# Kernel optimization log

Hardware: AMD Instinct MI355X
Metric: run time of the kernel (lower is better)

## Reference

```python
import jax, jax.numpy as jnp
import numpy as np

NEG = -1e7  # matches replace_masked value -10000000.0


def tree_lstm(x, graph, wx, bx, uh, bh):
    # x: (B,T,I); graph: (B,T,T); wx: (4,H,I) gates [i,f,o,u]; uh: (4,H,H)
    B, T, _ = x.shape
    H = wx.shape[1]
    # precompute input projections for all gates/timesteps: (B,T,4,H)
    xg = jnp.einsum('bti,ghi->btgh', x, wx) + bx[None, None]
    h0 = jnp.zeros((B, T, H), x.dtype)

    def step(carry, j):
        h, c = carry
        h_j = h[:, j]  # still zeros at step j, as in the original code
        i = jax.nn.sigmoid(xg[:, j, 0] + h_j @ uh[0].T + bh[0])
        o = jax.nn.sigmoid(xg[:, j, 2] + h_j @ uh[2].T + bh[2])
        u = jnp.tanh(xg[:, j, 3] + h_j @ uh[3].T + bh[3])
        # forget gate against every node's hidden state: (B,T,H)
        f = jax.nn.sigmoid(xg[:, j, 1][:, None, :] + h @ uh[1].T + bh[1])
        # masked neighbor aggregation: bmm(mask, f*c) with mask row j
        c_j = i * u + jnp.einsum('bt,bth->bh', graph[:, j], f * c)
        h_j_new = o * jnp.tanh(c_j)
        return (h.at[:, j].set(h_j_new), c.at[:, j].set(c_j)), None

    (h, c), _ = jax.lax.scan(step, (h0, jnp.zeros_like(h0)), jnp.arange(T))
    return h, c


def masked_softmax(scores, key_mask):
    # scores: (B,Q,K); key_mask: (B,K)
    scores = jnp.where(key_mask[:, None, :] > 0, scores, NEG)
    return jax.nn.softmax(scores, axis=-1)


def pool(v, mask):
    avg = jnp.sum(v * mask[:, :, None], axis=1) / jnp.sum(mask, axis=1, keepdims=True)
    mx = jnp.max(jnp.where(mask[:, :, None] > 0, v, NEG), axis=1)
    return avg, mx


def esim_forward(premises, premises_lengths, hypotheses, hypotheses_lengths,
                 lgraph, rgraph, emb,
                 enc_wx, enc_bx, enc_uh, enc_bh,
                 comp_wx, comp_bx, comp_uh, comp_bh,
                 proj_w, proj_b, cls_w1, cls_b1, cls_w2, cls_b2):
    Tp = premises.shape[1]
    Th = hypotheses.shape[1]
    p_mask = (jnp.arange(Tp)[None, :] < premises_lengths[:, None]).astype(emb.dtype)
    h_mask = (jnp.arange(Th)[None, :] < hypotheses_lengths[:, None]).astype(emb.dtype)

    emb_p = emb[premises]
    emb_h = emb[hypotheses]

    enc_p, _ = tree_lstm(emb_p, lgraph, enc_wx, enc_bx, enc_uh, enc_bh)
    enc_h, _ = tree_lstm(emb_h, rgraph, enc_wx, enc_bx, enc_uh, enc_bh)

    # soft alignment attention
    sim = jnp.einsum('bph,bqh->bpq', enc_p, enc_h)
    att_p = masked_softmax(sim, h_mask) @ enc_h                      # (B,Tp,H)
    att_h = masked_softmax(sim.transpose(0, 2, 1), p_mask) @ enc_p   # (B,Th,H)

    enh_p = jnp.concatenate([enc_p, att_p, enc_p - att_p, enc_p * att_p], axis=-1)
    enh_h = jnp.concatenate([enc_h, att_h, enc_h - att_h, enc_h * att_h], axis=-1)

    proj_p = jax.nn.relu(enh_p @ proj_w.T + proj_b)
    proj_h = jax.nn.relu(enh_h @ proj_w.T + proj_b)

    v_ai, _ = tree_lstm(proj_p, lgraph, comp_wx, comp_bx, comp_uh, comp_bh)
    v_bj, _ = tree_lstm(proj_h, rgraph, comp_wx, comp_bx, comp_uh, comp_bh)

    a_avg, a_max = pool(v_ai, p_mask)
    b_avg, b_max = pool(v_bj, h_mask)
    v = jnp.concatenate([a_avg, a_max, b_avg, b_max], axis=1)

    hid = jnp.tanh(v @ cls_w1.T + cls_b1)
    logits = hid @ cls_w2.T + cls_b2
    return logits


def setup_inputs() -> dict:
    B, T, E, H, V, C = 32, 128, 300, 300, 50000, 3
    key = jax.random.key(0)
    ks = jax.random.split(key, 20)
    premises = jax.random.randint(ks[0], (B, T), 1, V)
    premises_lengths = jax.random.randint(ks[1], (B,), T // 2, T + 1)
    hypotheses = jax.random.randint(ks[2], (B, T), 1, V)
    hypotheses_lengths = jax.random.randint(ks[3], (B,), T // 2, T + 1)
    # sparse binary adjacency (~1-2 children per node), as in dependency trees
    lgraph = (jax.random.uniform(ks[4], (B, T, T)) < 0.01).astype(jnp.float32)
    rgraph = (jax.random.uniform(ks[5], (B, T, T)) < 0.01).astype(jnp.float32)
    emb = jax.random.normal(ks[6], (V, E), jnp.float32) * 0.05
    emb = emb.at[0].set(0.0)  # padding_idx=0

    def g(k, shape, fan_in):
        return jax.random.normal(k, shape, jnp.float32) * (1.0 / np.sqrt(fan_in))

    return {
        'premises': premises, 'premises_lengths': premises_lengths,
        'hypotheses': hypotheses, 'hypotheses_lengths': hypotheses_lengths,
        'lgraph': lgraph, 'rgraph': rgraph, 'emb': emb,
        'enc_wx': g(ks[7], (4, H, E), E), 'enc_bx': jnp.zeros((4, H), jnp.float32),
        'enc_uh': g(ks[8], (4, H, H), H), 'enc_bh': jnp.zeros((4, H), jnp.float32),
        'comp_wx': g(ks[9], (4, H, H), H), 'comp_bx': jnp.zeros((4, H), jnp.float32),
        'comp_uh': g(ks[10], (4, H, H), H), 'comp_bh': jnp.zeros((4, H), jnp.float32),
        'proj_w': g(ks[11], (H, 4 * H), 4 * H), 'proj_b': jnp.zeros((H,), jnp.float32),
        'cls_w1': g(ks[12], (H, 4 * H), 4 * H), 'cls_b1': jnp.zeros((H,), jnp.float32),
        'cls_w2': g(ks[13], (C, H), H), 'cls_b2': jnp.zeros((C,), jnp.float32),
    }


def reference(premises, premises_lengths, hypotheses, hypotheses_lengths,
              lgraph, rgraph, emb,
              enc_wx, enc_bx, enc_uh, enc_bh,
              comp_wx, comp_bx, comp_uh, comp_bh,
              proj_w, proj_b, cls_w1, cls_b1, cls_w2, cls_b2):
    return esim_forward(premises, premises_lengths, hypotheses, hypotheses_lengths,
                        lgraph, rgraph, emb,
                        enc_wx, enc_bx, enc_uh, enc_bh,
                        comp_wx, comp_bx, comp_uh, comp_bh,
                        proj_w, proj_b, cls_w1, cls_b1, cls_w2, cls_b2)
```

## Files before the change

kernel.cpp:

```cpp
#include <hip/hip_runtime.h>
#include <math.h>

#define B_ 32
#define T_ 128
#define H_ 300
#define HG 1200
#define LMAX 10
#define WLCAP 8192
#define ECAP 2048
#define NEGV -10000000.0f

typedef __attribute__((ext_vector_type(8))) short bf16x8;
typedef __attribute__((ext_vector_type(4))) float f32x4;
typedef unsigned short ushort_t;

__device__ __forceinline__ float sigm(float x){ return 1.f/(1.f+expf(-x)); }

__device__ __forceinline__ unsigned short f2bf(float x){
  union { float f; unsigned int u; } c; c.f = x;
  unsigned int u = c.u;
  return (unsigned short)((u + 0x7fffu + ((u >> 16) & 1u)) >> 16);
}
__device__ __forceinline__ float bf2f(unsigned short h){
  union { unsigned int u; float f; } c; c.u = ((unsigned int)h) << 16;
  return c.f;
}

__global__ __launch_bounds__(256) void k_prep_all(
    const float* __restrict__ enc_uh, const float* __restrict__ comp_uh,
    const float* __restrict__ enc_wx, const float* __restrict__ comp_wx,
    const float* __restrict__ pw, const float* __restrict__ cw1,
    float* __restrict__ te, float* __restrict__ tc, float* __restrict__ w1t,
    ushort_t* __restrict__ WencH, ushort_t* __restrict__ WencL,
    ushort_t* __restrict__ WcompH, ushort_t* __restrict__ WcompL,
    ushort_t* __restrict__ WPH, ushort_t* __restrict__ WPL)
{
  int i = blockIdx.x*256 + threadIdx.x;
  if (i < 90000) {
    int m = i / H_, k = i - m*H_;
    te[i] = enc_uh[H_*H_ + (size_t)k*H_ + m];
    tc[i] = comp_uh[H_*H_ + (size_t)k*H_ + m];
  } else if (i < 450000) {
    int i2 = i - 90000;
    int m = i2 / H_, k = i2 - m*H_;
    w1t[i2] = cw1[(size_t)k*HG + m];
  } else if (i < 834000) {
    int i2 = i - 450000;
    int n = i2 / 320, k = i2 - n*320;
    float v = (k < 300) ? enc_wx[(size_t)n*300 + k] : 0.f;
    ushort_t h = f2bf(v);
    WencH[i2] = h; WencL[i2] = f2bf(v - bf2f(h));
  } else if (i < 1218000) {
    int i2 = i - 834000;
    int n = i2 / 320, k = i2 - n*320;
    float v = (k < 300) ? comp_wx[(size_t)n*300 + k] : 0.f;
    ushort_t h = f2bf(v);
    WcompH[i2] = h; WcompL[i2] = f2bf(v - bf2f(h));
  } else if (i < 1496400) {
    int i2 = i - 1218000;
    int n = i2 / 928, k = i2 - n*928;
    const float* r = pw + (size_t)n*HG;
    float v = 0.f;
    if (k < 300)      v = r[k] + r[600+k];
    else if (k < 600) v = r[k] - r[k+300];
    else if (k < 900) v = r[k+300];
    ushort_t h = f2bf(v);
    WPH[i2] = h; WPL[i2] = f2bf(v - bf2f(h));
  }
}

__global__ __launch_bounds__(256) void k_embed_split(const int* __restrict__ prem, const int* __restrict__ hyp,
    const float* __restrict__ emb, ushort_t* __restrict__ EH, ushort_t* __restrict__ EL)
{
  int i = blockIdx.x*256 + threadIdx.x;
  int bt = i / 320, k = i - bt*320;
  int side = bt >> 12, bt2 = bt & 4095;
  float v = 0.f;
  if (k < 300) {
    int tok = (side == 0 ? prem : hyp)[bt2];
    v = emb[(size_t)tok*H_ + k];
  }
  ushort_t h = f2bf(v);
  EH[i] = h; EL[i] = f2bf(v - bf2f(h));
}

__global__ __launch_bounds__(256) void k_h_split(const float* __restrict__ H1,
    ushort_t* __restrict__ HH, ushort_t* __restrict__ HL)
{
  int i = blockIdx.x*256 + threadIdx.x;
  int r = i / 320, k = i - r*320;
  float v = (k < 300) ? H1[(size_t)r*H_ + k] : 0.f;
  ushort_t h = f2bf(v);
  HH[i] = h; HL[i] = f2bf(v - bf2f(h));
}

__global__ __launch_bounds__(256) void k_enh_split(const float* __restrict__ H1, const float* __restrict__ ATT,
    ushort_t* __restrict__ AH, ushort_t* __restrict__ AL)
{
  int i = blockIdx.x*256 + threadIdx.x;
  int r = i / 928, k = i - r*928;
  float v = 0.f;
  if (k < 300)      v = H1[(size_t)r*H_ + k];
  else if (k < 600) v = ATT[(size_t)r*H_ + k - 300];
  else if (k < 900) { int kk = k - 600; v = H1[(size_t)r*H_ + kk] * ATT[(size_t)r*H_ + kk]; }
  ushort_t h = f2bf(v);
  AH[i] = h; AL[i] = f2bf(v - bf2f(h));
}

__global__ __launch_bounds__(256) void k_build(const float* __restrict__ lg, const float* __restrict__ rg,
    int* __restrict__ cnt_g, int* __restrict__ coff_g, int* __restrict__ eidx_g, float* __restrict__ ew_g,
    int* __restrict__ hasp_g, int* __restrict__ depth_g, int* __restrict__ maxd_g,
    int* __restrict__ lvlcnt_g, int* __restrict__ wl_g)
{
  int chain = blockIdx.x; int s = chain >> 5, b = chain & 31;
  const float* graph = (s ? rg : lg) + (size_t)b*T_*T_;
  int tid = threadIdx.x;
  __shared__ float gbuf[T_*T_];
  __shared__ int cnt[T_], coff[T_], depth[T_], hasp[T_];
  __shared__ short eidx[ECAP];
  __shared__ float ew[ECAP];
  __shared__ int lcnt[LMAX], lbase[LMAX], lppos[LMAX], lnpos[LMAX];
  __shared__ int etot_s;

  #pragma unroll
  for (int k = 0; k < 16; ++k)
    ((float4*)gbuf)[tid + k*256] = ((const float4*)graph)[tid + k*256];
  if (tid < T_) hasp[tid] = 0;
  if (tid < LMAX) { lcnt[tid] = 0; lppos[tid] = 0; lnpos[tid] = 0; }
  __syncthreads();
  if (tid < T_) {
    int j = tid, c = 0;
    const float* gr = gbuf + j*T_;
    for (int t = 0; t < j; ++t) c += (gr[t] != 0.f) ? 1 : 0;
    cnt[j] = c;
  }
  __syncthreads();
  if (tid == 0) { int a = 0; for (int j = 0; j < T_; ++j) { coff[j] = a; a += cnt[j]; } etot_s = a; }
  __syncthreads();
  if (tid < T_) {
    int j = tid, p = coff[j];
    const float* gr = gbuf + j*T_;
    for (int t = 0; t < j; ++t) {
      float g = gr[t];
      if (g != 0.f && p < ECAP) { eidx[p] = (short)t; ew[p] = g; hasp[t] = 1; ++p; }
    }
  }
  __syncthreads();
  if (tid == 0) {
    int md = 0;
    for (int j = 0; j < T_; ++j) {
      int d = 0, e0 = coff[j], e1 = coff[j] + cnt[j];
      if (e1 > ECAP) e1 = ECAP;
      for (int k = e0; k < e1; ++k) { int dd = depth[eidx[k]] + 1; d = dd > d ? dd : d; }
      depth[j] = d; md = d > md ? d : md;
    }
    maxd_g[chain] = md;
  }
  __syncthreads();
  if (tid < T_) { int L = depth[tid]; if (L < LMAX) atomicAdd(&lcnt[L], 1); }
  __syncthreads();
  if (tid < LMAX && lcnt[tid] > 0) lbase[tid] = atomicAdd(&lvlcnt_g[tid], lcnt[tid]);
  __syncthreads();
  if (tid < T_) {
    int L = depth[tid];
    if (L < LMAX) {
      int pos;
      if (hasp[tid]) { int p = atomicAdd(&lppos[L], 1); pos = p; }
      else           { int p = atomicAdd(&lnpos[L], 1); pos = lcnt[L] - 1 - p; }
      wl_g[L*WLCAP + lbase[L] + pos] = (chain << 8) | tid;
    }
  }
  int base = chain * T_;
  if (tid < T_) {
    cnt_g[base+tid] = cnt[tid]; coff_g[base+tid] = coff[tid];
    hasp_g[base+tid] = hasp[tid]; depth_g[base+tid] = depth[tid];
  }
  int etot = etot_s; if (etot > ECAP) etot = ECAP;
  for (int i = tid; i < etot; i += 256) { eidx_g[chain*ECAP + i] = eidx[i]; ew_g[chain*ECAP + i] = ew[i]; }
}

__global__ __launch_bounds__(1024) void k_level(
    const float* __restrict__ xg, const float* __restrict__ bhv, const float* __restrict__ uh1T,
    const int* __restrict__ cnt_g, const int* __restrict__ coff_g,
    const int* __restrict__ eidx_g, const float* __restrict__ ew_g,
    const int* __restrict__ hasp_g, const int* __restrict__ lvlcnt_g, const int* __restrict__ wl_g,
    int L, float* __restrict__ hout, float* __restrict__ chist, float* __restrict__ fh)
{
  int count = lvlcnt_g[L];
  int nblk = (count + 3) >> 2;
  int tid = threadIdx.x;
  __shared__ float h_s[4][H_];
  __shared__ float psum[3][4][H_];
  __shared__ int nodes[4];
  __shared__ int anyp;
  for (int blk = blockIdx.x; blk < nblk; blk += gridDim.x) {
    int base = blk * 4;
    int nn = count - base; if (nn > 4) nn = 4;
    if (tid == 0) anyp = 0;
    __syncthreads();
    if (tid < 4) {
      int pk = (tid < nn) ? wl_g[L*WLCAP + base + tid] : -1;
      nodes[tid] = pk;
      if (pk >= 0 && hasp_g[(pk >> 8)*T_ + (pk & 255)]) atomicAdd(&anyp, 1);
    }
    __syncthreads();
    for (int w = tid; w < nn*H_; w += 1024) {
      int n = w / H_, e = w - n*H_;
      int pk = nodes[n]; int chain = pk >> 8, j = pk & 255;
      size_t cb = (size_t)chain*T_*H_, xb = (size_t)chain*T_*HG;
      const float* xp = xg + xb + (size_t)j*HG;
      float x0 = xp[e], x1 = xp[H_+e], x2 = xp[2*H_+e], x3 = xp[3*H_+e];
      float iu  = sigm(x0 + bhv[e]) * tanhf(x3 + bhv[3*H_+e]);
      float og  = sigm(x2 + bhv[2*H_+e]);
      float x1b = x1 + bhv[H_+e];
      float acc = iu;
      int c0 = coff_g[chain*T_+j], c1 = c0 + cnt_g[chain*T_+j];
      const int* ei = eidx_g + chain*ECAP;
      const float* ewp = ew_g + chain*ECAP;
      for (int k = c0; k < c1; ++k) {
        int t = ei[k];
        acc += ewp[k] * sigm(x1b + fh[cb + (size_t)t*H_ + e]) * chist[cb + (size_t)t*H_ + e];
      }
      chist[cb + (size_t)j*H_ + e] = acc;
      float hv = og * tanhf(acc);
      hout[cb + (size_t)j*H_ + e] = hv;
      h_s[n][e] = hv;
    }
    __syncthreads();
    if (anyp > 0) {
      if (tid < 3*H_) {
        int g = tid / H_, e = tid - g*H_;
        float a0=0.f, a1=0.f, a2=0.f, a3=0.f;
        const float* up = uh1T + e;
        int m0 = g*100, m1 = m0 + 100;
        #pragma unroll 4
        for (int m = m0; m < m1; ++m) {
          float u = up[(size_t)m*H_];
          a0 = fmaf(u, h_s[0][m], a0);
          a1 = fmaf(u, h_s[1][m], a1);
          a2 = fmaf(u, h_s[2][m], a2);
          a3 = fmaf(u, h_s[3][m], a3);
        }
        psum[g][0][e]=a0; psum[g][1][e]=a1; psum[g][2][e]=a2; psum[g][3][e]=a3;
      }
      __syncthreads();
      for (int w = tid; w < nn*H_; w += 1024) {
        int n = w / H_, e = w - n*H_;
        int pk = nodes[n]; int chain = pk >> 8, j = pk & 255;
        if (hasp_g[chain*T_+j]) {
          size_t cb = (size_t)chain*T_*H_;
          fh[cb + (size_t)j*H_ + e] = psum[0][n][e] + psum[1][n][e] + psum[2][n][e];
        }
      }
    }
    __syncthreads();
  }
}

__global__ __launch_bounds__(320) void k_tail(const float* __restrict__ xg, const float* __restrict__ bhv,
    const float* __restrict__ uh1T, const int* __restrict__ cnt_g, const int* __restrict__ coff_g,
    const int* __restrict__ eidx_g, const float* __restrict__ ew_g, const int* __restrict__ hasp_g,
    const int* __restrict__ depth_g, const int* __restrict__ maxd_g,
    float* __restrict__ hout, float* __restrict__ chist, float* __restrict__ fh)
{
  int chain = blockIdx.x;
  if (maxd_g[chain] < LMAX) return;
  int tid = threadIdx.x;
  bool act = tid < H_;
  float bh0=0.f,bh1=0.f,bh2=0.f,bh3=0.f;
  if (act) { bh0=bhv[tid]; bh1=bhv[H_+tid]; bh2=bhv[2*H_+tid]; bh3=bhv[3*H_+tid]; }
  __shared__ float h_lds[H_];
  size_t cb = (size_t)chain*T_*H_, xb = (size_t)chain*T_*HG;
  const int* ei = eidx_g + chain*ECAP;
  const float* ewp = ew_g + chain*ECAP;
  for (int j = 0; j < T_; ++j) {
    if (depth_g[chain*T_+j] < LMAX) continue;
    if (act) {
      const float* xp = xg + xb + (size_t)j*HG;
      float x0 = xp[tid], x1 = xp[H_+tid], x2 = xp[2*H_+tid], x3 = xp[3*H_+tid];
      float acc = sigm(x0+bh0) * tanhf(x3+bh3);
      float og  = sigm(x2+bh2);
      float x1b = x1 + bh1;
      int c0 = coff_g[chain*T_+j], c1 = c0 + cnt_g[chain*T_+j];
      for (int k = c0; k < c1; ++k) {
        int t = ei[k];
        acc += ewp[k] * sigm(x1b + fh[cb + (size_t)t*H_ + tid]) * chist[cb + (size_t)t*H_ + tid];
      }
      chist[cb + (size_t)j*H_ + tid] = acc;
      float hv = og * tanhf(acc);
      hout[cb + (size_t)j*H_ + tid] = hv;
      h_lds[tid] = hv;
    }
    __syncthreads();
    if (hasp_g[chain*T_+j] && act) {
      float a = 0.f;
      const float* up = uh1T + tid;
      #pragma unroll 4
      for (int m = 0; m < H_; ++m) a = fmaf(up[(size_t)m*H_], h_lds[m], a);
      fh[cb + (size_t)j*H_ + tid] = a;
    }
    __syncthreads();
  }
}

template<int OUTBF>
__global__ __launch_bounds__(256) void k_gemm_bf(
    const ushort_t* __restrict__ Ah, const ushort_t* __restrict__ Al, int AS,
    const ushort_t* __restrict__ Wh, const ushort_t* __restrict__ Wl, int WS,
    const float* __restrict__ bias, float* __restrict__ C,
    ushort_t* __restrict__ Ch, ushort_t* __restrict__ Cl, int CS,
    int N, int NT, int act)
{
  __shared__ ushort_t sAh[128*32], sAl[128*32], sWh[128*32], sWl[128*32];
  int tid = threadIdx.x;
  int bn = blockIdx.x * 128, bm = blockIdx.y * 128;
  int lane = tid & 63, wave = tid >> 6;
  int wr = (wave >> 1) * 64, wc = (wave & 1) * 64;
  int lrow = lane & 15, q = lane >> 4;

  int srow = tid >> 1, half = tid & 1;
  int ssw = (srow >> 1) & 3;
  int sg0 = ((2*half) ^ ssw) * 8, sg1 = ((2*half+1) ^ ssw) * 8;
  int sbase = srow * 32;
  const ushort_t* pAh = Ah + (size_t)(bm + srow)*AS + half*16;
  const ushort_t* pAl = Al + (size_t)(bm + srow)*AS + half*16;
  int wrow = bn + srow;
  int wsafe = (wrow < N) ? wrow : 0;
  const ushort_t* pWh = Wh + (size_t)wsafe*WS + half*16;
  const ushort_t* pWl = Wl + (size_t)wsafe*WS + half*16;

  bf16x8 rA0, rA1, rAl0, rAl1, rW0, rW1, rWl0, rWl1;
  auto issue = [&](int t){
    int kb = t * 32;
    rA0  = *(const bf16x8*)(pAh + kb); rA1  = *(const bf16x8*)(pAh + kb + 8);
    rAl0 = *(const bf16x8*)(pAl + kb); rAl1 = *(const bf16x8*)(pAl + kb + 8);
    rW0  = *(const bf16x8*)(pWh + kb); rW1  = *(const bf16x8*)(pWh + kb + 8);
    rWl0 = *(const bf16x8*)(pWl + kb); rWl1 = *(const bf16x8*)(pWl + kb + 8);
  };
  auto commit = [&](){
    *(bf16x8*)&sAh[sbase + sg0] = rA0; *(bf16x8*)&sAh[sbase + sg1] = rA1;
    *(bf16x8*)&sAl[sbase + sg0] = rAl0; *(bf16x8*)&sAl[sbase + sg1] = rAl1;
    *(bf16x8*)&sWh[sbase + sg0] = rW0; *(bf16x8*)&sWh[sbase + sg1] = rW1;
    *(bf16x8*)&sWl[sbase + sg0] = rWl0; *(bf16x8*)&sWl[sbase + sg1] = rWl1;
  };

  f32x4 acc[4][4];
  #pragma unroll
  for (int m = 0; m < 4; ++m)
    #pragma unroll
    for (int n = 0; n < 4; ++n) acc[m][n] = (f32x4){0.f,0.f,0.f,0.f};

  issue(0); commit();
  __syncthreads();
  for (int t = 0; t < NT; ++t) {
    bool more = (t+1 < NT);
    if (more) issue(t+1);
    bf16x8 ah[4], al[4], bh[4], bl[4];
    #pragma unroll
    for (int m = 0; m < 4; ++m) {
      int R = wr + m*16 + lrow;
      int o = R*32 + ((q ^ ((R>>1)&3)) * 8);
      ah[m] = *(const bf16x8*)&sAh[o];
      al[m] = *(const bf16x8*)&sAl[o];
    }
    #pragma unroll
    for (int n = 0; n < 4; ++n) {
      int R = wc + n*16 + lrow;
      int o = R*32 + ((q ^ ((R>>1)&3)) * 8);
      bh[n] = *(const bf16x8*)&sWh[o];
      bl[n] = *(const bf16x8*)&sWl[o];
    }
    #pragma unroll
    for (int m = 0; m < 4; ++m)
      #pragma unroll
      for (int n = 0; n < 4; ++n) {
        acc[m][n] = __builtin_amdgcn_mfma_f32_16x16x32_bf16(ah[m], bh[n], acc[m][n], 0,0,0);
        acc[m][n] = __builtin_amdgcn_mfma_f32_16x16x32_bf16(ah[m], bl[n], acc[m][n], 0,0,0);
        acc[m][n] = __builtin_amdgcn_mfma_f32_16x16x32_bf16(al[m], bh[n], acc[m][n], 0,0,0);
      }
    __syncthreads();
    if (more) commit();
    __syncthreads();
  }
  #pragma unroll
  for (int m = 0; m < 4; ++m) {
    int row0 = bm + wr + m*16 + (lane >> 4)*4;
    #pragma unroll
    for (int n = 0; n < 4; ++n) {
      int col = bn + wc + n*16 + lrow;
      if (OUTBF) {
        if (col < CS) {
          float bv = (col < N) ? bias[col] : 0.f;
          #pragma unroll
          for (int r = 0; r < 4; ++r) {
            float v = 0.f;
            if (col < N) { v = acc[m][n][r] + bv; if (act) v = fmaxf(v, 0.f); }
            ushort_t h = f2bf(v);
            Ch[(size_t)(row0 + r)*CS + col] = h;
            Cl[(size_t)(row0 + r)*CS + col] = f2bf(v - bf2f(h));
          }
        }
      } else {
        if (col < N) {
          float bv = bias[col];
          #pragma unroll
          for (int r = 0; r < 4; ++r) {
            float v = acc[m][n][r] + bv;
            if (act) v = fmaxf(v, 0.f);
            C[(size_t)(row0 + r)*N + col] = v;
          }
        }
      }
    }
  }
}

__global__ __launch_bounds__(256) void k_attn_mfma(
    const ushort_t* __restrict__ HH, const ushort_t* __restrict__ HL,
    const int* __restrict__ plen, const int* __restrict__ hlen,
    float* __restrict__ ATT)
{
  __shared__ float regA_f[12800];
  __shared__ ushort_t pbuf[2*64*136];
  ushort_t* regA = (ushort_t*)regA_f;

  int tid = threadIdx.x;
  int lane = tid & 63, wave = tid >> 6;
  int lrow = lane & 15, koff = (lane >> 4) * 8;
  int d = blockIdx.x, b = blockIdx.y, q0 = blockIdx.z * 64;
  int qbase = (d*B_ + b)*T_ + q0;
  int kbase = ((1-d)*B_ + b)*T_;
  float* outp = ATT + ((size_t)(d*B_ + b)*T_ + q0) * H_;
  int klen = (d == 0) ? hlen[b] : plen[b];

  ushort_t* sQh = regA;
  ushort_t* sQl = regA + 2560;
  ushort_t* sKh = regA + 5120;
  ushort_t* sKl = regA + 10240;
  int qrow = tid >> 2, qo = (tid & 3) * 8;
  int krow = tid >> 1, ko = (tid & 1) * 16;
  const ushort_t* Qh = HH + (size_t)(qbase + qrow)*320 + qo;
  const ushort_t* Ql = HL + (size_t)(qbase + qrow)*320 + qo;
  const ushort_t* Kh = HH + (size_t)(kbase + krow)*320 + ko;
  const ushort_t* Kl = HL + (size_t)(kbase + krow)*320 + ko;

  bf16x8 rqh, rql, rkh0, rkh1, rkl0, rkl1;
  auto issue1 = [&](int t){
    int kb = t*32;
    rqh  = *(const bf16x8*)(Qh + kb);
    rql  = *(const bf16x8*)(Ql + kb);
    rkh0 = *(const bf16x8*)(Kh + kb); rkh1 = *(const bf16x8*)(Kh + kb + 8);
    rkl0 = *(const bf16x8*)(Kl + kb); rkl1 = *(const bf16x8*)(Kl + kb + 8);
  };
  auto commit1 = [&](){
    *(bf16x8*)&sQh[qrow*40 + qo] = rqh;
    *(bf16x8*)&sQl[qrow*40 + qo] = rql;
    *(bf16x8*)&sKh[krow*40 + ko] = rkh0; *(bf16x8*)&sKh[krow*40 + ko + 8] = rkh1;
    *(bf16x8*)&sKl[krow*40 + ko] = rkl0; *(bf16x8*)&sKl[krow*40 + ko + 8] = rkl1;
  };

  f32x4 acc1[4][2];
  #pragma unroll
  for (int m = 0; m < 4; ++m)
    #pragma unroll
    for (int n = 0; n < 2; ++n) acc1[m][n] = (f32x4){0.f,0.f,0.f,0.f};
  int wc = wave * 32;

  issue1(0); commit1();
  __syncthreads();
  for (int t = 0; t < 10; ++t) {
    bool more = (t < 9);
    bf16x8 ah[4], al[4], bh[2], bl[2];
    #pragma unroll
    for (int m = 0; m < 4; ++m) {
      int o = (m*16 + lrow)*40 + koff;
      ah[m] = *(const bf16x8*)&sQh[o];
      al[m] = *(const bf16x8*)&sQl[o];
    }
    #pragma unroll
    for (int n = 0; n < 2; ++n) {
      int o = (wc + n*16 + lrow)*40 + koff;
      bh[n] = *(const bf16x8*)&sKh[o];
      bl[n] = *(const bf16x8*)&sKl[o];
    }
    if (more) issue1(t+1);
    __syncthreads();
    if (more) commit1();
    #pragma unroll
    for (int m = 0; m < 4; ++m)
      #pragma unroll
      for (int n = 0; n < 2; ++n) {
        acc1[m][n] = __builtin_amdgcn_mfma_f32_16x16x32_bf16(ah[m], bh[n], acc1[m][n], 0,0,0);
        acc1[m][n] = __builtin_amdgcn_mfma_f32_16x16x32_bf16(ah[m], bl[n], acc1[m][n], 0,0,0);
        acc1[m][n] = __builtin_amdgcn_mfma_f32_16x16x32_bf16(al[m], bh[n], acc1[m][n], 0,0,0);
      }
    __syncthreads();
  }
  float* sim = regA_f;
  #pragma unroll
  for (int m = 0; m < 4; ++m)
    #pragma unroll
    for (int n = 0; n < 2; ++n)
      #pragma unroll
      for (int r = 0; r < 4; ++r)
        sim[(m*16 + (lane>>4)*4 + r)*132 + wc + n*16 + lrow] = acc1[m][n][r];
  __syncthreads();

  {
    int row = tid >> 2, qtr = (tid & 3) * 32;
    const float* sr = sim + row*132;
    float mx = NEGV;
    for (int c = 0; c < 32; ++c) { int cg = qtr + c; float s = (cg < klen) ? sr[cg] : NEGV; mx = fmaxf(mx, s); }
    mx = fmaxf(mx, __shfl_xor(mx, 1));
    mx = fmaxf(mx, __shfl_xor(mx, 2));
    float sum = 0.f;
    for (int c = 0; c < 32; ++c) { int cg = qtr + c; if (cg < klen) sum += expf(sr[cg] - mx); }
    sum += __shfl_xor(sum, 1);
    sum += __shfl_xor(sum, 2);
    float rinv = 1.f / sum;
    for (int c = 0; c < 32; ++c) {
      int cg = qtr + c;
      float p = (cg < klen) ? expf(sr[cg] - mx) * rinv : 0.f;
      ushort_t h = f2bf(p);
      pbuf[row*136 + cg] = h;
      pbuf[64*136 + row*136 + cg] = f2bf(p - bf2f(h));
    }
  }
  __syncthreads();

  ushort_t* kth = regA;
  ushort_t* ktl = regA + 12800;
  int wr2 = (wave & 1) * 32;
  int wcf = (wave >> 1) * 160;
  f32x4 acc3[2][10];
  #pragma unroll
  for (int m = 0; m < 2; ++m)
    #pragma unroll
    for (int n = 0; n < 10; ++n) acc3[m][n] = (f32x4){0.f,0.f,0.f,0.f};
  int skey = tid >> 3, sf8 = tid & 7;

  for (int kc = 0; kc < 4; ++kc) {
    __syncthreads();
    int key = kbase + kc*32 + skey;
    const ushort_t* krh = HH + (size_t)key*320;
    const ushort_t* krl = HL + (size_t)key*320;
    for (int f8 = sf8; f8 < 40; f8 += 8) {
      bf16x8 vh = *(const bf16x8*)(krh + f8*8);
      bf16x8 vl = *(const bf16x8*)(krl + f8*8);
      #pragma unroll
      for (int i = 0; i < 8; ++i) {
        int feat = f8*8 + i;
        kth[feat*40 + skey] = (ushort_t)vh[i];
        ktl[feat*40 + skey] = (ushort_t)vl[i];
      }
    }
    __syncthreads();
    bf16x8 ph[2], pl[2], kh[10], kl[10];
    #pragma unroll
    for (int m = 0; m < 2; ++m) {
      int o = (wr2 + m*16 + lrow)*136 + kc*32 + koff;
      ph[m] = *(const bf16x8*)&pbuf[o];
      pl[m] = *(const bf16x8*)&pbuf[64*136 + o];
    }
    #pragma unroll
    for (int n = 0; n < 10; ++n) {
      int o = (wcf + n*16 + lrow)*40 + koff;
      kh[n] = *(const bf16x8*)&kth[o];
      kl[n] = *(const bf16x8*)&ktl[o];
    }
    #pragma unroll
    for (int m = 0; m < 2; ++m)
      #pragma unroll
      for (int n = 0; n < 10; ++n) {
        acc3[m][n] = __builtin_amdgcn_mfma_f32_16x16x32_bf16(ph[m], kh[n], acc3[m][n], 0,0,0);
        acc3[m][n] = __builtin_amdgcn_mfma_f32_16x16x32_bf16(ph[m], kl[n], acc3[m][n], 0,0,0);
        acc3[m][n] = __builtin_amdgcn_mfma_f32_16x16x32_bf16(pl[m], kh[n], acc3[m][n], 0,0,0);
      }
  }
  #pragma unroll
  for (int m = 0; m < 2; ++m) {
    int row0 = wr2 + m*16 + (lane >> 4)*4;
    #pragma unroll
    for (int n = 0; n < 10; ++n) {
      int col = wcf + n*16 + lrow;
      if (col < H_) {
        #pragma unroll
        for (int r = 0; r < 4; ++r)
          outp[(size_t)(row0 + r)*H_ + col] = acc3[m][n][r];
      }
    }
  }
}

__global__ __launch_bounds__(320) void k_pool(const float* __restrict__ H,
    const int* __restrict__ plen, const int* __restrict__ hlen,
    float* __restrict__ psum, float* __restrict__ pmax)
{
  int chain = blockIdx.x; int s = chain >> 5, b = chain & 31;
  int c = blockIdx.y; int t0 = c * 16;
  int len = (s == 0 ? plen[b] : hlen[b]);
  int tid = threadIdx.x;
  __shared__ float buf[16*H_];
  const float* hp = H + (size_t)chain*T_*H_ + (size_t)t0*H_;
  for (int i = tid; i < 16*H_; i += 320) buf[i] = hp[i];
  __syncthreads();
  if (tid < H_) {
    int tmax = len - t0; if (tmax > 16) tmax = 16;
    float sum = 0.f, mx = NEGV;
    for (int t = 0; t < tmax; ++t) { float x = buf[t*H_ + tid]; sum += x; mx = fmaxf(mx, x); }
    int o = (chain*8 + c)*H_ + tid;
    psum[o] = sum; pmax[o] = mx;
  }
}

__global__ __launch_bounds__(320) void k_classify(
    const float* __restrict__ psum, const float* __restrict__ pmax,
    const int* __restrict__ plen, const int* __restrict__ hlen,
    const float* __restrict__ w1t, const float* __restrict__ b1,
    const float* __restrict__ w2, const float* __restrict__ b2,
    float* __restrict__ out)
{
  int b = blockIdx.x;
  int tid = threadIdx.x;
  __shared__ float v[HG];
  __shared__ float hid[H_];
  for (int s = 0; s < 2; ++s) {
    int chain = s*B_ + b;
    int len = (s == 0 ? plen[b] : hlen[b]);
    if (tid < H_) {
      float sum = 0.f, mx = NEGV;
      #pragma unroll
      for (int c = 0; c < 8; ++c) {
        int o = (chain*8 + c)*H_ + tid;
        sum += psum[o]; mx = fmaxf(mx, pmax[o]);
      }
      v[s*600 + tid]       = sum / (float)len;
      v[s*600 + 300 + tid] = mx;
    }
  }
  __syncthreads();
  if (tid < H_) {
    float a0 = b1[tid], a1 = 0.f, a2 = 0.f, a3 = 0.f;
    for (int m = 0; m < HG; m += 4) {
      a0 = fmaf(v[m+0], w1t[(size_t)(m+0)*H_ + tid], a0);
      a1 = fmaf(v[m+1], w1t[(size_t)(m+1)*H_ + tid], a1);
      a2 = fmaf(v[m+2], w1t[(size_t)(m+2)*H_ + tid], a2);
      a3 = fmaf(v[m+3], w1t[(size_t)(m+3)*H_ + tid], a3);
    }
    hid[tid] = tanhf(a0 + a1 + a2 + a3);
  }
  __syncthreads();
  if (tid < 3) {
    float a = b2[tid];
    const float* wr = w2 + (size_t)tid*H_;
    for (int n = 0; n < H_; ++n) a = fmaf(hid[n], wr[n], a);
    out[b*3 + tid] = a;
  }
}

extern "C" void kernel_launch(void* const* d_in, const int* in_sizes, int n_in,
                              void* d_out, int out_size, void* d_ws, size_t ws_size,
                              hipStream_t stream) {
  const int*   prem    = (const int*)d_in[0];
  const int*   plen    = (const int*)d_in[1];
  const int*   hyp     = (const int*)d_in[2];
  const int*   hlen    = (const int*)d_in[3];
  const float* lg      = (const float*)d_in[4];
  const float* rg      = (const float*)d_in[5];
  const float* emb     = (const float*)d_in[6];
  const float* enc_wx  = (const float*)d_in[7];
  const float* enc_bx  = (const float*)d_in[8];
  const float* enc_uh  = (const float*)d_in[9];
  const float* enc_bh  = (const float*)d_in[10];
  const float* comp_wx = (const float*)d_in[11];
  const float* comp_bx = (const float*)d_in[12];
  const float* comp_uh = (const float*)d_in[13];
  const float* comp_bh = (const float*)d_in[14];
  const float* proj_w  = (const float*)d_in[15];
  const float* proj_b  = (const float*)d_in[16];
  const float* cls_w1  = (const float*)d_in[17];
  const float* cls_b1  = (const float*)d_in[18];
  const float* cls_w2  = (const float*)d_in[19];
  const float* cls_b2  = (const float*)d_in[20];
  float* outp = (float*)d_out;

  float* XG  = (float*)d_ws;
  ushort_t* EH = (ushort_t*)(XG + 9830400);
  ushort_t* EL = EH + 2621440;
  float* H1  = XG + 9830400 + 2621440;
  float* CH  = H1 + 2457600;
  float* FH  = CH + 2457600;
  float* UTE = FH + 2457600;
  float* UTC = UTE + 90000;
  float* W1T = UTC + 90000;
  ushort_t* WencH  = (ushort_t*)(W1T + 360000);
  ushort_t* WencL  = WencH + 384000;
  ushort_t* WcompH = WencL + 384000;
  ushort_t* WcompL = WcompH + 384000;
  ushort_t* WPH    = WcompL + 384000;
  ushort_t* WPL    = WPH + 278400;
  float* PSUM = W1T + 360000 + 1046400;
  float* PMAX = PSUM + 153600;
  float* EW   = PMAX + 153600;
  int* EIDX   = (int*)(EW + 64*ECAP);
  int* CNT    = EIDX + 64*ECAP;
  int* COFF   = CNT + 64*T_;
  int* DEPTH  = COFF + 64*T_;
  int* HASP   = DEPTH + 64*T_;
  int* MAXD   = HASP + 64*T_;
  int* LVLCNT = MAXD + 64;
  int* WL     = LVLCNT + LMAX;
  float* ATT  = CH;
  ushort_t* ENH_H = (ushort_t*)XG;
  ushort_t* ENH_L = ENH_H + 7602176;

  hipMemsetAsync(LVLCNT, 0, LMAX*sizeof(int), stream);
  k_prep_all<<<(1496400 + 255)/256, 256, 0, stream>>>(enc_uh, comp_uh, enc_wx, comp_wx, proj_w, cls_w1,
      UTE, UTC, W1T, WencH, WencL, WcompH, WcompL, WPH, WPL);
  k_build<<<64, 256, 0, stream>>>(lg, rg, CNT, COFF, EIDX, EW, HASP, DEPTH, MAXD, LVLCNT, WL);
  k_embed_split<<<10240, 256, 0, stream>>>(prem, hyp, emb, EH, EL);
  k_gemm_bf<0><<<dim3(10, 64), 256, 0, stream>>>(EH, EL, 320, WencH, WencL, 320,
      enc_bx, XG, nullptr, nullptr, 0, HG, 10, 0);
  for (int L = 0; L < LMAX; ++L)
    k_level<<<640, 1024, 0, stream>>>(XG, enc_bh, UTE, CNT, COFF, EIDX, EW, HASP, LVLCNT, WL, L, H1, CH, FH);
  k_tail<<<64, 320, 0, stream>>>(XG, enc_bh, UTE, CNT, COFF, EIDX, EW, HASP, DEPTH, MAXD, H1, CH, FH);
  k_h_split<<<10240, 256, 0, stream>>>(H1, EH, EL);
  k_attn_mfma<<<dim3(2, B_, 2), 256, 0, stream>>>(EH, EL, plen, hlen, ATT);
  k_enh_split<<<29696, 256, 0, stream>>>(H1, ATT, ENH_H, ENH_L);
  k_gemm_bf<1><<<dim3(3, 64), 256, 0, stream>>>(ENH_H, ENH_L, 928, WPH, WPL, 928,
      proj_b, nullptr, EH, EL, 320, H_, 29, 1);
  k_gemm_bf<0><<<dim3(10, 64), 256, 0, stream>>>(EH, EL, 320, WcompH, WcompL, 320,
      comp_bx, XG, nullptr, nullptr, 0, HG, 10, 0);
  for (int L = 0; L < LMAX; ++L)
    k_level<<<640, 1024, 0, stream>>>(XG, comp_bh, UTC, CNT, COFF, EIDX, EW, HASP, LVLCNT, WL, L, H1, CH, FH);
  k_tail<<<64, 320, 0, stream>>>(XG, comp_bh, UTC, CNT, COFF, EIDX, EW, HASP, DEPTH, MAXD, H1, CH, FH);
  k_pool<<<dim3(64, 8), 320, 0, stream>>>(H1, plen, hlen, PSUM, PMAX);
  k_classify<<<B_, 320, 0, stream>>>(PSUM, PMAX, plen, hlen, W1T, cls_b1, cls_w2, cls_b2, outp);
}
```

Before: 495.4 us.

## Cap level-parallel tree depth and double-buffer register prefetch in bf16 GEMM

```diff
diff --git a/kernel.cpp b/kernel.cpp
--- a/kernel.cpp
+++ b/kernel.cpp
@@ -5,7 +5,7 @@
 #define T_ 128
 #define H_ 300
 #define HG 1200
-#define LMAX 10
+#define TAILD 4
 #define WLCAP 8192
 #define ECAP 2048
 #define NEGV -10000000.0f
@@ -119,14 +119,14 @@
   __shared__ int cnt[T_], coff[T_], depth[T_], hasp[T_];
   __shared__ short eidx[ECAP];
   __shared__ float ew[ECAP];
-  __shared__ int lcnt[LMAX], lbase[LMAX], lppos[LMAX], lnpos[LMAX];
+  __shared__ int lcnt[TAILD], lbase[TAILD], lppos[TAILD], lnpos[TAILD];
   __shared__ int etot_s;
 
   #pragma unroll
   for (int k = 0; k < 16; ++k)
     ((float4*)gbuf)[tid + k*256] = ((const float4*)graph)[tid + k*256];
   if (tid < T_) hasp[tid] = 0;
-  if (tid < LMAX) { lcnt[tid] = 0; lppos[tid] = 0; lnpos[tid] = 0; }
+  if (tid < TAILD) { lcnt[tid] = 0; lppos[tid] = 0; lnpos[tid] = 0; }
   __syncthreads();
   if (tid < T_) {
     int j = tid, c = 0;
@@ -157,13 +157,13 @@
     maxd_g[chain] = md;
   }
   __syncthreads();
-  if (tid < T_) { int L = depth[tid]; if (L < LMAX) atomicAdd(&lcnt[L], 1); }
-  __syncthreads();
-  if (tid < LMAX && lcnt[tid] > 0) lbase[tid] = atomicAdd(&lvlcnt_g[tid], lcnt[tid]);
+  if (tid < T_) { int L = depth[tid]; if (L < TAILD) atomicAdd(&lcnt[L], 1); }
+  __syncthreads();
+  if (tid < TAILD && lcnt[tid] > 0) lbase[tid] = atomicAdd(&lvlcnt_g[tid], lcnt[tid]);
   __syncthreads();
   if (tid < T_) {
     int L = depth[tid];
-    if (L < LMAX) {
+    if (L < TAILD) {
       int pos;
       if (hasp[tid]) { int p = atomicAdd(&lppos[L], 1); pos = p; }
       else           { int p = atomicAdd(&lnpos[L], 1); pos = lcnt[L] - 1 - p; }
@@ -264,7 +264,7 @@
     float* __restrict__ hout, float* __restrict__ chist, float* __restrict__ fh)
 {
   int chain = blockIdx.x;
-  if (maxd_g[chain] < LMAX) return;
+  if (maxd_g[chain] < TAILD) return;
   int tid = threadIdx.x;
   bool act = tid < H_;
   float bh0=0.f,bh1=0.f,bh2=0.f,bh3=0.f;
@@ -274,7 +274,7 @@
   const int* ei = eidx_g + chain*ECAP;
   const float* ewp = ew_g + chain*ECAP;
   for (int j = 0; j < T_; ++j) {
-    if (depth_g[chain*T_+j] < LMAX) continue;
+    if (depth_g[chain*T_+j] < TAILD) continue;
     if (act) {
       const float* xp = xg + xb + (size_t)j*HG;
       float x0 = xp[tid], x1 = xp[H_+tid], x2 = xp[2*H_+tid], x3 = xp[3*H_+tid];
@@ -303,13 +303,13 @@
   }
 }
 
-template<int OUTBF>
+template<int OUTBF, int NT>
 __global__ __launch_bounds__(256) void k_gemm_bf(
     const ushort_t* __restrict__ Ah, const ushort_t* __restrict__ Al, int AS,
     const ushort_t* __restrict__ Wh, const ushort_t* __restrict__ Wl, int WS,
     const float* __restrict__ bias, float* __restrict__ C,
     ushort_t* __restrict__ Ch, ushort_t* __restrict__ Cl, int CS,
-    int N, int NT, int act)
+    int N, int act)
 {
   __shared__ ushort_t sAh[128*32], sAl[128*32], sWh[128*32], sWl[128*32];
   int tid = threadIdx.x;
@@ -329,20 +329,19 @@
   const ushort_t* pWh = Wh + (size_t)wsafe*WS + half*16;
   const ushort_t* pWl = Wl + (size_t)wsafe*WS + half*16;
 
-  bf16x8 rA0, rA1, rAl0, rAl1, rW0, rW1, rWl0, rWl1;
-  auto issue = [&](int t){
-    int kb = t * 32;
-    rA0  = *(const bf16x8*)(pAh + kb); rA1  = *(const bf16x8*)(pAh + kb + 8);
-    rAl0 = *(const bf16x8*)(pAl + kb); rAl1 = *(const bf16x8*)(pAl + kb + 8);
-    rW0  = *(const bf16x8*)(pWh + kb); rW1  = *(const bf16x8*)(pWh + kb + 8);
-    rWl0 = *(const bf16x8*)(pWl + kb); rWl1 = *(const bf16x8*)(pWl + kb + 8);
-  };
-  auto commit = [&](){
-    *(bf16x8*)&sAh[sbase + sg0] = rA0; *(bf16x8*)&sAh[sbase + sg1] = rA1;
-    *(bf16x8*)&sAl[sbase + sg0] = rAl0; *(bf16x8*)&sAl[sbase + sg1] = rAl1;
-    *(bf16x8*)&sWh[sbase + sg0] = rW0; *(bf16x8*)&sWh[sbase + sg1] = rW1;
-    *(bf16x8*)&sWl[sbase + sg0] = rWl0; *(bf16x8*)&sWl[sbase + sg1] = rWl1;
-  };
+  bf16x8 aA0,aA1,aA2,aA3,aW0,aW1,aW2,aW3;
+  bf16x8 bA0,bA1,bA2,bA3,bW0,bW1,bW2,bW3;
+
+#define ISSUE_SET(P,t) { int kb = (t)*32; \
+    P##A0 = *(const bf16x8*)(pAh + kb); P##A1 = *(const bf16x8*)(pAh + kb + 8); \
+    P##A2 = *(const bf16x8*)(pAl + kb); P##A3 = *(const bf16x8*)(pAl + kb + 8); \
+    P##W0 = *(const bf16x8*)(pWh + kb); P##W1 = *(const bf16x8*)(pWh + kb + 8); \
+    P##W2 = *(const bf16x8*)(pWl + kb); P##W3 = *(const bf16x8*)(pWl + kb + 8); }
+#define COMMIT_SET(P) { \
+    *(bf16x8*)&sAh[sbase + sg0] = P##A0; *(bf16x8*)&sAh[sbase + sg1] = P##A1; \
+    *(bf16x8*)&sAl[sbase + sg0] = P##A2; *(bf16x8*)&sAl[sbase + sg1] = P##A3; \
+    *(bf16x8*)&sWh[sbase + sg0] = P##W0; *(bf16x8*)&sWh[sbase + sg1] = P##W1; \
+    *(bf16x8*)&sWl[sbase + sg0] = P##W2; *(bf16x8*)&sWl[sbase + sg1] = P##W3; }
 
   f32x4 acc[4][4];
   #pragma unroll
@@ -350,38 +349,53 @@
     #pragma unroll
     for (int n = 0; n < 4; ++n) acc[m][n] = (f32x4){0.f,0.f,0.f,0.f};
 
-  issue(0); commit();
-  __syncthreads();
-  for (int t = 0; t < NT; ++t) {
-    bool more = (t+1 < NT);
-    if (more) issue(t+1);
-    bf16x8 ah[4], al[4], bh[4], bl[4];
-    #pragma unroll
-    for (int m = 0; m < 4; ++m) {
-      int R = wr + m*16 + lrow;
-      int o = R*32 + ((q ^ ((R>>1)&3)) * 8);
-      ah[m] = *(const bf16x8*)&sAh[o];
-      al[m] = *(const bf16x8*)&sAl[o];
-    }
-    #pragma unroll
-    for (int n = 0; n < 4; ++n) {
-      int R = wc + n*16 + lrow;
-      int o = R*32 + ((q ^ ((R>>1)&3)) * 8);
-      bh[n] = *(const bf16x8*)&sWh[o];
-      bl[n] = *(const bf16x8*)&sWl[o];
-    }
-    #pragma unroll
-    for (int m = 0; m < 4; ++m)
-      #pragma unroll
-      for (int n = 0; n < 4; ++n) {
-        acc[m][n] = __builtin_amdgcn_mfma_f32_16x16x32_bf16(ah[m], bh[n], acc[m][n], 0,0,0);
-        acc[m][n] = __builtin_amdgcn_mfma_f32_16x16x32_bf16(ah[m], bl[n], acc[m][n], 0,0,0);
-        acc[m][n] = __builtin_amdgcn_mfma_f32_16x16x32_bf16(al[m], bh[n], acc[m][n], 0,0,0);
-      }
-    __syncthreads();
-    if (more) commit();
-    __syncthreads();
-  }
+#define FRAG_MFMA() { \
+    bf16x8 ah[4], al[4], bh[4], bl[4]; \
+    _Pragma("unroll") \
+    for (int m = 0; m < 4; ++m) { \
+      int R = wr + m*16 + lrow; \
+      int o = R*32 + ((q ^ ((R>>1)&3)) * 8); \
+      ah[m] = *(const bf16x8*)&sAh[o]; \
+      al[m] = *(const bf16x8*)&sAl[o]; \
+    } \
+    _Pragma("unroll") \
+    for (int n = 0; n < 4; ++n) { \
+      int R = wc + n*16 + lrow; \
+      int o = R*32 + ((q ^ ((R>>1)&3)) * 8); \
+      bh[n] = *(const bf16x8*)&sWh[o]; \
+      bl[n] = *(const bf16x8*)&sWl[o]; \
+    } \
+    _Pragma("unroll") \
+    for (int m = 0; m < 4; ++m) \
+      _Pragma("unroll") \
+      for (int n = 0; n < 4; ++n) { \
+        acc[m][n] = __builtin_amdgcn_mfma_f32_16x16x32_bf16(ah[m], bh[n], acc[m][n], 0,0,0); \
+        acc[m][n] = __builtin_amdgcn_mfma_f32_16x16x32_bf16(ah[m], bl[n], acc[m][n], 0,0,0); \
+        acc[m][n] = __builtin_amdgcn_mfma_f32_16x16x32_bf16(al[m], bh[n], acc[m][n], 0,0,0); \
+      } }
+
+  ISSUE_SET(a, 0); COMMIT_SET(a);
+  __syncthreads();
+  if (NT > 1) ISSUE_SET(b, 1);
+  #pragma unroll
+  for (int t = 0; t < NT; t += 2) {
+    FRAG_MFMA();
+    if (t+2 < NT) ISSUE_SET(a, t+2);
+    __syncthreads();
+    if (t+1 < NT) COMMIT_SET(b);
+    __syncthreads();
+    if (t+1 < NT) {
+      FRAG_MFMA();
+      if (t+3 < NT) ISSUE_SET(b, t+3);
+      __syncthreads();
+      if (t+2 < NT) COMMIT_SET(a);
+      __syncthreads();
+    }
+  }
+#undef ISSUE_SET
+#undef COMMIT_SET
+#undef FRAG_MFMA
+
   #pragma unroll
   for (int m = 0; m < 4; ++m) {
     int row0 = bm + wr + m*16 + (lane >> 4)*4;
@@ -709,29 +723,29 @@
   int* HASP   = DEPTH + 64*T_;
   int* MAXD   = HASP + 64*T_;
   int* LVLCNT = MAXD + 64;
-  int* WL     = LVLCNT + LMAX;
+  int* WL     = LVLCNT + TAILD;
   float* ATT  = CH;
   ushort_t* ENH_H = (ushort_t*)XG;
   ushort_t* ENH_L = ENH_H + 7602176;
 
-  hipMemsetAsync(LVLCNT, 0, LMAX*sizeof(int), stream);
+  hipMemsetAsync(LVLCNT, 0, TAILD*sizeof(int), stream);
   k_prep_all<<<(1496400 + 255)/256, 256, 0, stream>>>(enc_uh, comp_uh, enc_wx, comp_wx, proj_w, cls_w1,
       UTE, UTC, W1T, WencH, WencL, WcompH, WcompL, WPH, WPL);
   k_build<<<64, 256, 0, stream>>>(lg, rg, CNT, COFF, EIDX, EW, HASP, DEPTH, MAXD, LVLCNT, WL);
   k_embed_split<<<10240, 256, 0, stream>>>(prem, hyp, emb, EH, EL);
-  k_gemm_bf<0><<<dim3(10, 64), 256, 0, stream>>>(EH, EL, 320, WencH, WencL, 320,
-      enc_bx, XG, nullptr, nullptr, 0, HG, 10, 0);
-  for (int L = 0; L < LMAX; ++L)
+  k_gemm_bf<0,10><<<dim3(10, 64), 256, 0, stream>>>(EH, EL, 320, WencH, WencL, 320,
+      enc_bx, XG, nullptr, nullptr, 0, HG, 0);
+  for (int L = 0; L < TAILD; ++L)
     k_level<<<640, 1024, 0, stream>>>(XG, enc_bh, UTE, CNT, COFF, EIDX, EW, HASP, LVLCNT, WL, L, H1, CH, FH);
   k_tail<<<64, 320, 0, stream>>>(XG, enc_bh, UTE, CNT, COFF, EIDX, EW, HASP, DEPTH, MAXD, H1, CH, FH);
   k_h_split<<<10240, 256, 0, stream>>>(H1, EH, EL);
   k_attn_mfma<<<dim3(2, B_, 2), 256, 0, stream>>>(EH, EL, plen, hlen, ATT);
   k_enh_split<<<29696, 256, 0, stream>>>(H1, ATT, ENH_H, ENH_L);
-  k_gemm_bf<1><<<dim3(3, 64), 256, 0, stream>>>(ENH_H, ENH_L, 928, WPH, WPL, 928,
-      proj_b, nullptr, EH, EL, 320, H_, 29, 1);
-  k_gemm_bf<0><<<dim3(10, 64), 256, 0, stream>>>(EH, EL, 320, WcompH, WcompL, 320,
-      comp_bx, XG, nullptr, nullptr, 0, HG, 10, 0);
-  for (int L = 0; L < LMAX; ++L)
+  k_gemm_bf<1,29><<<dim3(3, 64), 256, 0, stream>>>(ENH_H, ENH_L, 928, WPH, WPL, 928,
+      proj_b, nullptr, EH, EL, 320, H_, 1);
+  k_gemm_bf<0,10><<<dim3(10, 64), 256, 0, stream>>>(EH, EL, 320, WcompH, WcompL, 320,
+      comp_bx, XG, nullptr, nullptr, 0, HG, 0);
+  for (int L = 0; L < TAILD; ++L)
     k_level<<<640, 1024, 0, stream>>>(XG, comp_bh, UTC, CNT, COFF, EIDX, EW, HASP, LVLCNT, WL, L, H1, CH, FH);
   k_tail<<<64, 320, 0, stream>>>(XG, comp_bh, UTC, CNT, COFF, EIDX, EW, HASP, DEPTH, MAXD, H1, CH, FH);
   k_pool<<<dim3(64, 8), 320, 0, stream>>>(H1, plen, hlen, PSUM, PMAX);
```

After: 492.4 us. Within noise of the previous version (-0.6%).
